# Performance work log

Hardware: AMD Instinct MI355X
Metric: run time of the kernel (lower is better)

The kernel has to match this reference:

```python
import jax, jax.numpy as jnp
import numpy as np

SEG = 2048      # segment_length
RATE = 4        # dilated_rate
DIM = 768
LN_EPS = 1e-5


def _sparsify(x):
    # b (l s) d -> b l s d, take every RATE-th within segment, flatten back
    b, L, d = x.shape
    x = x.reshape(b, L // SEG, SEG, d)[:, :, ::RATE]
    return x.reshape(b, -1, d)


def _layernorm(x, gamma, beta):
    mu = jnp.mean(x, axis=-1, keepdims=True)
    var = jnp.mean(jnp.square(x - mu), axis=-1, keepdims=True)
    return (x - mu) / jnp.sqrt(var + LN_EPS) * gamma + beta


def setup_inputs() -> dict:
    key = jax.random.key(0)
    ks = jax.random.split(key, 6)
    B, L, D = 4, 8192, DIM
    return {
        "Q": jax.random.normal(ks[0], (B, L, D), dtype=jnp.float32),
        "K": jax.random.normal(ks[1], (B, L, D), dtype=jnp.float32),
        "V": jax.random.normal(ks[2], (B, L, D), dtype=jnp.float32),
        "Wq": jax.random.normal(ks[3], (D, D), dtype=jnp.float32) * (1.0 / np.sqrt(D)),
        "Wk": jax.random.normal(ks[4], (D, D), dtype=jnp.float32) * (1.0 / np.sqrt(D)),
        "Wv": jax.random.normal(ks[5], (D, D), dtype=jnp.float32) * (1.0 / np.sqrt(D)),
        "ln_gamma": jnp.ones((D,), dtype=jnp.float32),
        "ln_beta": jnp.zeros((D,), dtype=jnp.float32),
    }


def reference(Q, K, V, Wq, Wk, Wv, ln_gamma, ln_beta):
    # strided segment dilation gather
    q = _sparsify(Q)  # [B, Ls, D], Ls = L/SEG * ceil(SEG/RATE)
    k = _sparsify(K)
    v = _sparsify(V)
    # linear projections (torch Linear: y = x @ W.T, no bias)
    q = q @ Wq.T
    k = k @ Wk.T
    v = v @ Wv.T
    # qk LayerNorm (shared norm module)
    q = _layernorm(q, ln_gamma, ln_beta)
    k = _layernorm(k, ln_gamma, ln_beta)
    # scaled dot product attention (non-causal, default scale 1/sqrt(D))
    scale = 1.0 / np.sqrt(q.shape[-1]).astype(np.float32)
    attn = jax.nn.softmax(jnp.einsum('bqd,bkd->bqk', q, k) * scale, axis=-1)
    out = jnp.einsum('bqk,bkd->bqd', attn, v)
    # dropout is identity in eval mode; final softmax over feature dim (as in source)
    return jax.nn.softmax(out, axis=-1)
```

## Files before the change

### kernel.cpp

```cpp
#include <hip/hip_runtime.h>
#include <math.h>

#define SEGLEN 2048
#define SRATE 4
#define DIM 768
#define BATCH 4
#define LFULL 8192
#define LSP 2048
#define NROWS (BATCH * LSP)
#define LN_EPS 1e-5f
#define ATT_SCALE 0.03608439182435161f

typedef __attribute__((ext_vector_type(8))) short s16x8;
typedef __attribute__((ext_vector_type(4))) float f32x4;

__device__ __forceinline__ ushort f2bf(float f) {
    unsigned u = __float_as_uint(f);
    u += 0x7fffu + ((u >> 16) & 1u);
    return (ushort)(u >> 16);
}
__device__ __forceinline__ float bf2f(ushort h) {
    return __uint_as_float(((unsigned)h) << 16);
}

__device__ __forceinline__ void ld_lds16(const ushort* g, ushort* l) {
    __builtin_amdgcn_global_load_lds(
        (const __attribute__((address_space(1))) void*)g,
        (__attribute__((address_space(3))) void*)l, 16, 0, 0);
}

__global__ void pack3(const float* __restrict__ Q, const float* __restrict__ Ks,
                      const float* __restrict__ V, ushort* __restrict__ X) {
    const float* src = blockIdx.z == 0 ? Q : blockIdx.z == 1 ? Ks : V;
    ushort* dst = X + (long)blockIdx.z * (NROWS * DIM);
    int idx = blockIdx.x * 256 + threadIdx.x;
    int r  = idx / (DIM / 4);
    int dg = idx - r * (DIM / 4);
    int bb = r >> 11;
    int s  = r & 2047;
    int seg = s >> 9;
    int j   = s & 511;
    long srow = (long)bb * LFULL + seg * SEGLEN + j * SRATE;
    float4 f = *(const float4*)(src + srow * DIM + dg * 4);
    ushort4 o;
    o.x = f2bf(f.x); o.y = f2bf(f.y); o.z = f2bf(f.z); o.w = f2bf(f.w);
    *(ushort4*)(dst + (long)r * DIM + dg * 4) = o;
}

__global__ void conv3(const float* __restrict__ Wq, const float* __restrict__ Wk,
                      const float* __restrict__ Wv, ushort* __restrict__ W) {
    const float* src = blockIdx.z == 0 ? Wq : blockIdx.z == 1 ? Wk : Wv;
    ushort* dst = W + (long)blockIdx.z * (DIM * DIM);
    int idx = blockIdx.x * 256 + threadIdx.x;
    float4 f = *(const float4*)(src + (long)idx * 4);
    ushort4 o;
    o.x = f2bf(f.x); o.y = f2bf(f.y); o.z = f2bf(f.z); o.w = f2bf(f.w);
    *(ushort4*)(dst + (long)idx * 4) = o;
}

#define GTILE 128
#define GBK 32

template<int MODE>
__global__ __launch_bounds__(256) void gemm_bt(
    const ushort* __restrict__ Ag, const ushort* __restrict__ Bg,
    ushort* __restrict__ Cb, ushort* __restrict__ Cb2,
    float* __restrict__ Cf, float* __restrict__ Cf2, float* __restrict__ lsum,
    int M, int N, int K, int lda, int ldb, long sA, long sB, long sC,
    int ldc, float scale)
{
    __shared__ ushort As[GTILE * GBK];
    __shared__ ushort Bs[GTILE * GBK];

    const int z = blockIdx.z;
    const int bz = (MODE == 3) ? (z >> 1) : z;
    const int hz = (MODE == 3) ? (z & 1) : 0;
    const ushort* A = Ag + (long)bz * sA + (long)hz * K;
    const ushort* B = Bg + (long)bz * sB + (long)hz * K;

    const int tid = threadIdx.x;
    const int rowBase = blockIdx.y * GTILE;
    const int colBase = blockIdx.x * GTILE;
    const int wid = tid >> 6, lane = tid & 63;
    const int wm = wid >> 1, wn = wid & 1;
    const int quad = lane >> 4, lr = lane & 15;

    f32x4 acc[4][4] = {};

    const ushort* gA = A + (long)(rowBase + wid * 32 + (lane >> 2)) * lda + (lane & 3) * 8;
    const ushort* gB = B + (long)(colBase + wid * 32 + (lane >> 2)) * ldb + (lane & 3) * 8;
    ushort* lA = As + wid * 1024;
    ushort* lB = Bs + wid * 1024;

    for (int k0 = 0; k0 < K; k0 += GBK) {
        __syncthreads();
        ld_lds16(gA + k0, lA);
        ld_lds16(gA + 16 * lda + k0, lA + 512);
        ld_lds16(gB + k0, lB);
        ld_lds16(gB + 16 * ldb + k0, lB + 512);
        __syncthreads();

        s16x8 af[4], bfm[4];
#pragma unroll
        for (int t = 0; t < 4; t++)
            af[t] = *(const s16x8*)&As[(wm * 64 + t * 16 + lr) * GBK + quad * 8];
#pragma unroll
        for (int t = 0; t < 4; t++)
            bfm[t] = *(const s16x8*)&Bs[(wn * 64 + t * 16 + lr) * GBK + quad * 8];
#pragma unroll
        for (int i = 0; i < 4; i++)
#pragma unroll
            for (int j = 0; j < 4; j++)
                acc[i][j] = __builtin_amdgcn_mfma_f32_16x16x32_bf16(af[i], bfm[j], acc[i][j], 0, 0, 0);
    }

    if (MODE == 0) {
        if (z < 2) {
            ushort* Cz = Cb + (long)z * sC;
#pragma unroll
            for (int i = 0; i < 4; i++) {
                int r0 = rowBase + wm * 64 + i * 16 + quad * 4;
#pragma unroll
                for (int j = 0; j < 4; j++) {
                    int c = colBase + wn * 64 + j * 16 + lr;
#pragma unroll
                    for (int reg = 0; reg < 4; reg++)
                        Cz[(long)(r0 + reg) * ldc + c] = f2bf(acc[i][j][reg]);
                }
            }
        } else {
#pragma unroll
            for (int i = 0; i < 4; i++) {
                int r0 = rowBase + wm * 64 + i * 16 + quad * 4;
                int bidx = r0 >> 11;
                int jj = r0 & 2047;
                ushort* Cz = Cb2 + (long)bidx * DIM * LSP;
#pragma unroll
                for (int j = 0; j < 4; j++) {
                    int c = colBase + wn * 64 + j * 16 + lr;
                    ushort4 o;
                    o.x = f2bf(acc[i][j][0]); o.y = f2bf(acc[i][j][1]);
                    o.z = f2bf(acc[i][j][2]); o.w = f2bf(acc[i][j][3]);
                    *(ushort4*)(Cz + (long)c * LSP + jj) = o;
                }
            }
        }
    } else if (MODE == 2) {
        ushort* Cz = Cb + (long)z * sC;
        float* lz = lsum + (long)z * M;
#pragma unroll
        for (int i = 0; i < 4; i++) {
            int r0 = rowBase + wm * 64 + i * 16 + quad * 4;
#pragma unroll
            for (int reg = 0; reg < 4; reg++) {
                float s = 0.f;
#pragma unroll
                for (int j = 0; j < 4; j++) {
                    int c = colBase + wn * 64 + j * 16 + lr;
                    float e = __expf(acc[i][j][reg] * scale);
                    s += e;
                    Cz[(long)(r0 + reg) * ldc + c] = f2bf(e);
                }
                for (int m = 1; m < 16; m <<= 1) s += __shfl_xor(s, m, 64);
                if (lr == 0) atomicAdd(&lz[r0 + reg], s);
            }
        }
    } else {
        float* Cz = (hz ? Cf2 : Cf) + (long)bz * sC;
#pragma unroll
        for (int i = 0; i < 4; i++) {
            int r0 = rowBase + wm * 64 + i * 16 + quad * 4;
#pragma unroll
            for (int j = 0; j < 4; j++) {
                int c = colBase + wn * 64 + j * 16 + lr;
#pragma unroll
                for (int reg = 0; reg < 4; reg++)
                    Cz[(long)(r0 + reg) * ldc + c] = acc[i][j][reg];
            }
        }
    }
}

__global__ __launch_bounds__(256) void ln_inplace(
    ushort* __restrict__ X, const float* __restrict__ gamma,
    const float* __restrict__ beta)
{
    int wid = threadIdx.x >> 6, lane = threadIdx.x & 63;
    int row = blockIdx.x * 4 + wid;
    ushort* xp = X + (long)row * DIM;
    float v[12];
    float s = 0.f;
#pragma unroll
    for (int c = 0; c < 12; c++) { v[c] = bf2f(xp[c * 64 + lane]); s += v[c]; }
    for (int m = 1; m < 64; m <<= 1) s += __shfl_xor(s, m, 64);
    float mean = s * (1.0f / 768.0f);
    float q = 0.f;
#pragma unroll
    for (int c = 0; c < 12; c++) { float d = v[c] - mean; q += d * d; }
    for (int m = 1; m < 64; m <<= 1) q += __shfl_xor(q, m, 64);
    float rstd = rsqrtf(q * (1.0f / 768.0f) + LN_EPS);
#pragma unroll
    for (int c = 0; c < 12; c++) {
        int idx = c * 64 + lane;
        float y = (v[c] - mean) * rstd * gamma[idx] + beta[idx];
        xp[idx] = f2bf(y);
    }
}

__global__ __launch_bounds__(256) void final_softmax(
    const float* __restrict__ O0, const float* __restrict__ O1,
    const float* __restrict__ l, float* __restrict__ out)
{
    int wid = threadIdx.x >> 6, lane = threadIdx.x & 63;
    int row = blockIdx.x * 4 + wid;
    long base = (long)row * DIM;
    float inv = 1.0f / l[row];
    float v[12]; float mx = -1e30f;
#pragma unroll
    for (int c = 0; c < 12; c++) {
        v[c] = (O0[base + c * 64 + lane] + O1[base + c * 64 + lane]) * inv;
        mx = fmaxf(mx, v[c]);
    }
    for (int m = 1; m < 64; m <<= 1) mx = fmaxf(mx, __shfl_xor(mx, m, 64));
    float s = 0.f;
#pragma unroll
    for (int c = 0; c < 12; c++) { v[c] = __expf(v[c] - mx); s += v[c]; }
    for (int m = 1; m < 64; m <<= 1) s += __shfl_xor(s, m, 64);
    float invs = 1.0f / s;
#pragma unroll
    for (int c = 0; c < 12; c++) out[base + c * 64 + lane] = v[c] * invs;
}

extern "C" void kernel_launch(void* const* d_in, const int* in_sizes, int n_in,
                              void* d_out, int out_size, void* d_ws, size_t ws_size,
                              hipStream_t stream)
{
    const float* Q  = (const float*)d_in[0];
    const float* K_ = (const float*)d_in[1];
    const float* V  = (const float*)d_in[2];
    const float* Wq = (const float*)d_in[3];
    const float* Wk = (const float*)d_in[4];
    const float* Wv = (const float*)d_in[5];
    const float* g  = (const float*)d_in[6];
    const float* b  = (const float*)d_in[7];
    float* out = (float*)d_out;

    char* ws = (char*)d_ws;
    ushort* Xq  = (ushort*)(ws + 0);
    ushort* Wqb = (ushort*)(ws + 37748736);
    ushort* qb  = (ushort*)(ws + 41287680);
    ushort* kb  = (ushort*)(ws + 53870592);
    ushort* vT  = (ushort*)(ws + 66453504);
    float*  O0  = (float*)(ws + 79036416);
    float*  l   = (float*)(ws + 104202240);
    ushort* P   = (ushort*)(ws + 0);
    float*  O1  = (float*)(ws + 41287680);

    (void)in_sizes; (void)n_in; (void)out_size; (void)ws_size;

    hipMemsetAsync(l, 0, NROWS * sizeof(float), stream);

    pack3<<<dim3(6144, 1, 3), 256, 0, stream>>>(Q, K_, V, Xq);
    conv3<<<dim3(576, 1, 3), 256, 0, stream>>>(Wq, Wk, Wv, Wqb);

    gemm_bt<0><<<dim3(DIM / GTILE, NROWS / GTILE, 3), 256, 0, stream>>>(
        Xq, Wqb, qb, vT, nullptr, nullptr, nullptr,
        NROWS, DIM, DIM, DIM, DIM,
        (long)NROWS * DIM, (long)DIM * DIM, (long)NROWS * DIM, DIM, 0.f);

    ln_inplace<<<4096, 256, 0, stream>>>(qb, g, b);

    gemm_bt<2><<<dim3(LSP / GTILE, LSP / GTILE, BATCH), 256, 0, stream>>>(
        qb, kb, P, nullptr, nullptr, nullptr, l,
        LSP, LSP, DIM, DIM, DIM,
        (long)LSP * DIM, (long)LSP * DIM, (long)LSP * LSP, LSP, ATT_SCALE);

    gemm_bt<3><<<dim3(DIM / GTILE, LSP / GTILE, BATCH * 2), 256, 0, stream>>>(
        P, vT, nullptr, nullptr, O0, O1, nullptr,
        LSP, DIM, LSP / 2, LSP, LSP,
        (long)LSP * LSP, (long)DIM * LSP, (long)LSP * DIM, DIM, 0.f);

    final_softmax<<<2048, 256, 0, stream>>>(O0, O1, l, out);
}
```

Before: 424.6 us.

## Double GEMM K-tile, re-layout LDS staging, and remap block order across XCDs

Raises the GEMM K-step from 32 to 64 so each barrier pair covers twice as many MFMAs. It also changes the LDS staging layout: 8-row by 64-column chunks are stored so that fragment reads address 64-element groups, which likely cuts bank conflicts. A third change remaps the linearized block index with an 8-way interleave, so blocks that run on the same XCD handle contiguous tiles and share L2. In exchange, shared memory per block doubles, which may lower occupancy, and the remap assumes the total block count is divisible by 8.

```diff
diff --git a/kernel.cpp b/kernel.cpp
--- a/kernel.cpp
+++ b/kernel.cpp
@@ -59,7 +59,7 @@
 }
 
 #define GTILE 128
-#define GBK 32
+#define GBK 64
 
 template<int MODE>
 __global__ __launch_bounds__(256) void gemm_bt(
@@ -72,46 +72,61 @@
     __shared__ ushort As[GTILE * GBK];
     __shared__ ushort Bs[GTILE * GBK];
 
-    const int z = blockIdx.z;
+    const int CT = gridDim.x, RT = gridDim.y;
+    const int nt = CT * RT;
+    const int total = nt * gridDim.z;
+    int g = (blockIdx.z * RT + blockIdx.y) * CT + blockIdx.x;
+    g = (g & 7) * (total >> 3) + (g >> 3);
+    const int z = g / nt;
+    const int rem = g - z * nt;
+    const int by = rem / CT, bx = rem - by * CT;
+
     const int bz = (MODE == 3) ? (z >> 1) : z;
     const int hz = (MODE == 3) ? (z & 1) : 0;
     const ushort* A = Ag + (long)bz * sA + (long)hz * K;
     const ushort* B = Bg + (long)bz * sB + (long)hz * K;
 
     const int tid = threadIdx.x;
-    const int rowBase = blockIdx.y * GTILE;
-    const int colBase = blockIdx.x * GTILE;
+    const int rowBase = by * GTILE;
+    const int colBase = bx * GTILE;
     const int wid = tid >> 6, lane = tid & 63;
     const int wm = wid >> 1, wn = wid & 1;
     const int quad = lane >> 4, lr = lane & 15;
 
     f32x4 acc[4][4] = {};
 
-    const ushort* gA = A + (long)(rowBase + wid * 32 + (lane >> 2)) * lda + (lane & 3) * 8;
-    const ushort* gB = B + (long)(colBase + wid * 32 + (lane >> 2)) * ldb + (lane & 3) * 8;
-    ushort* lA = As + wid * 1024;
-    ushort* lB = Bs + wid * 1024;
+    const ushort* gA = A + (long)(rowBase + wid * 32 + (lane & 7)) * lda + (lane >> 3) * 8;
+    const ushort* gB = B + (long)(colBase + wid * 32 + (lane & 7)) * ldb + (lane >> 3) * 8;
+    ushort* lA = As + wid * 2048;
+    ushort* lB = Bs + wid * 2048;
+
+    const int fra = (wm * 8 + (lr >> 3)) * 512 + (lr & 7) * 8;
+    const int frb = (wn * 8 + (lr >> 3)) * 512 + (lr & 7) * 8;
 
     for (int k0 = 0; k0 < K; k0 += GBK) {
         __syncthreads();
-        ld_lds16(gA + k0, lA);
-        ld_lds16(gA + 16 * lda + k0, lA + 512);
-        ld_lds16(gB + k0, lB);
-        ld_lds16(gB + 16 * ldb + k0, lB + 512);
+#pragma unroll
+        for (int s = 0; s < 4; s++) {
+            ld_lds16(gA + (long)s * 8 * lda + k0, lA + s * 512);
+            ld_lds16(gB + (long)s * 8 * ldb + k0, lB + s * 512);
+        }
         __syncthreads();
 
-        s16x8 af[4], bfm[4];
-#pragma unroll
-        for (int t = 0; t < 4; t++)
-            af[t] = *(const s16x8*)&As[(wm * 64 + t * 16 + lr) * GBK + quad * 8];
-#pragma unroll
-        for (int t = 0; t < 4; t++)
-            bfm[t] = *(const s16x8*)&Bs[(wn * 64 + t * 16 + lr) * GBK + quad * 8];
-#pragma unroll
-        for (int i = 0; i < 4; i++)
-#pragma unroll
-            for (int j = 0; j < 4; j++)
-                acc[i][j] = __builtin_amdgcn_mfma_f32_16x16x32_bf16(af[i], bfm[j], acc[i][j], 0, 0, 0);
+#pragma unroll
+        for (int h = 0; h < 2; h++) {
+            s16x8 af[4], bfm[4];
+#pragma unroll
+            for (int t = 0; t < 4; t++)
+                af[t] = *(const s16x8*)&As[fra + t * 1024 + (h * 4 + quad) * 64];
+#pragma unroll
+            for (int t = 0; t < 4; t++)
+                bfm[t] = *(const s16x8*)&Bs[frb + t * 1024 + (h * 4 + quad) * 64];
+#pragma unroll
+            for (int i = 0; i < 4; i++)
+#pragma unroll
+                for (int j = 0; j < 4; j++)
+                    acc[i][j] = __builtin_amdgcn_mfma_f32_16x16x32_bf16(af[i], bfm[j], acc[i][j], 0, 0, 0);
+        }
     }
 
     if (MODE == 0) {
```

Result: slower. 460.1 us (+8.4%).
